# Performance work log

Hardware: AMD Instinct MI355X
Metric: run time of the kernel (lower is better)

## Reference

```python
import jax, jax.numpy as jnp
import numpy as np


def setup_inputs() -> dict:
    key = jax.random.key(0)
    k = jax.random.split(key, 4)
    B, F, E, U = 4096, 40, 64, 64
    return {
        "x": jax.random.normal(k[0], (B, F, E), dtype=jnp.float32),
        "attention_W": jax.random.normal(k[1], (E, U), dtype=jnp.float32) * (2.0 / (E + U)) ** 0.5,
        "attention_b": jnp.zeros((U,), dtype=jnp.float32),
        "projection_h": jax.random.normal(k[2], (U, 1), dtype=jnp.float32) * (2.0 / (U + 1)) ** 0.5,
        "projection_p": jax.random.normal(k[3], (E, 1), dtype=jnp.float32) * (2.0 / (E + 1)) ** 0.5,
    }


def reference(x, attention_W, attention_b, projection_h, projection_p):
    # x: [B, F, E] stacked field embeddings (original code takes a list of F [B,1,E])
    F = x.shape[1]
    ri, ci = np.triu_indices(F, k=1)  # static pair indices, P = F*(F-1)/2
    inner_product = x[:, ri, :] * x[:, ci, :]            # [B, P, E]
    attention_tmp = jax.nn.relu(
        jnp.einsum('bpe,eu->bpu', inner_product, attention_W) + attention_b
    )                                                    # [B, P, U]
    scores = jnp.einsum('bpu,uo->bpo', attention_tmp, projection_h)  # [B, P, 1]
    attention_weight = jax.nn.softmax(scores, axis=1)    # softmax over pairs
    attention_output = jnp.sum(inner_product * attention_weight, axis=1)  # [B, E]
    # dropout omitted (inference / eval mode)
    afm_out = attention_output @ projection_p            # [B, 1]
    return afm_out
```

## Files before the change

### kernel.cpp

```cpp
#include <hip/hip_runtime.h>
#include <hip/hip_fp16.h>

typedef _Float16 half8v __attribute__((ext_vector_type(8)));
typedef _Float16 half2v __attribute__((ext_vector_type(2)));
typedef float f32x4 __attribute__((ext_vector_type(4)));

#define DPP_XADD(x, ctrl)                                                          \
  x += __builtin_bit_cast(float, __builtin_amdgcn_mov_dpp(                         \
           __builtin_bit_cast(int, x), ctrl, 0xf, 0xf, true))

__global__ void afm_prep(const float* __restrict__ W, const float* __restrict__ pvec,
                         unsigned char* __restrict__ ws) {
  const int tid = threadIdx.x;
  _Float16* wf = (_Float16*)ws;
  _Float16* pf = (_Float16*)(ws + 8192);
  unsigned short* tbl = (unsigned short*)(ws + 10240);
  for (int idx = tid; idx < 4096; idx += 256) {
    int j = idx & 7, lane = (idx >> 3) & 63, nt = (idx >> 9) & 3, ks = idx >> 11;
    int k = ks * 32 + (lane >> 4) * 8 + j;
    int u = nt * 16 + (lane & 15);
    wf[idx] = (_Float16)W[k * 64 + u];
  }
  for (int idx = tid; idx < 1024; idx += 256) {
    int j = idx & 7, lane = (idx >> 3) & 63, ks = idx >> 9;
    int k = ks * 32 + (lane >> 4) * 8 + j;
    pf[idx] = ((lane & 15) == 0) ? (_Float16)pvec[k] : (_Float16)0.f;
  }
  for (int p = tid; p < 780; p += 256) {
    int i = 0, rem = p;
    while (rem >= 39 - i) { rem -= 39 - i; ++i; }
    int j = i + 1 + rem;
    tbl[p] = (unsigned short)((i << 8) | j);
  }
}

__global__ __launch_bounds__(256) void afm_main(
    const float* __restrict__ x, const float* __restrict__ bvec,
    const float* __restrict__ hvec, const unsigned char* __restrict__ ws,
    float* __restrict__ out) {
  __shared__ __align__(16) _Float16 xh[40 * 72];
  __shared__ __align__(16) unsigned short tbls[784];
  __shared__ float scs[784];
  __shared__ float s2s[784];
  __shared__ float red[12];

  const int tid = threadIdx.x;
  const int b = blockIdx.x;
  const int lane = tid & 63;
  const int wid = tid >> 6;

  const float4* xg = (const float4*)(x + b * 2560);
#pragma unroll
  for (int it = 0; it < 3; ++it) {
    int g = tid + it * 256;
    if (g < 640) {
      float4 v = xg[g];
      int f = g >> 4, e4 = g & 15;
      half2v* dst = (half2v*)&xh[f * 72 + e4 * 4];
      dst[0] = __builtin_bit_cast(half2v, __builtin_amdgcn_cvt_pkrtz(v.x, v.y));
      dst[1] = __builtin_bit_cast(half2v, __builtin_amdgcn_cvt_pkrtz(v.z, v.w));
    }
  }
  {
    const float4* tg = (const float4*)(ws + 10240);
    float4* ts = (float4*)tbls;
    if (tid < 98) ts[tid] = tg[tid];
  }
  const half8v* wfg = (const half8v*)ws;
  half8v wf[2][4];
#pragma unroll
  for (int ks = 0; ks < 2; ++ks)
#pragma unroll
    for (int nt = 0; nt < 4; ++nt) wf[ks][nt] = wfg[(ks * 4 + nt) * 64 + lane];
  const half8v* pfg = (const half8v*)(ws + 8192);
  half8v pf[2] = {pfg[lane], pfg[64 + lane]};
  float bu[4], hu[4];
#pragma unroll
  for (int nt = 0; nt < 4; ++nt) {
    int u = nt * 16 + (lane & 15);
    bu[nt] = bvec[u];
    hu[nt] = hvec[u];
  }
  __syncthreads();

  const int m = lane & 15, kg = lane >> 4;
  for (int t = wid; t < 49; t += 4) {
    int p = 16 * t + m;
    p = p > 779 ? 779 : p;
    unsigned pk = tbls[p];
    const _Float16* xi = &xh[(pk >> 8) * 72 + kg * 8];
    const _Float16* xj = &xh[(pk & 255) * 72 + kg * 8];
    half8v a0 = *(const half8v*)xi * *(const half8v*)xj;
    half8v a1 = *(const half8v*)(xi + 32) * *(const half8v*)(xj + 32);
    f32x4 acc[4], accp;
#pragma unroll
    for (int nt = 0; nt < 4; ++nt) acc[nt] = (f32x4){bu[nt], bu[nt], bu[nt], bu[nt]};
    accp = (f32x4){0.f, 0.f, 0.f, 0.f};
#pragma unroll
    for (int nt = 0; nt < 4; ++nt) {
      acc[nt] = __builtin_amdgcn_mfma_f32_16x16x32_f16(a0, wf[0][nt], acc[nt], 0, 0, 0);
      acc[nt] = __builtin_amdgcn_mfma_f32_16x16x32_f16(a1, wf[1][nt], acc[nt], 0, 0, 0);
    }
    accp = __builtin_amdgcn_mfma_f32_16x16x32_f16(a0, pf[0], accp, 0, 0, 0);
    accp = __builtin_amdgcn_mfma_f32_16x16x32_f16(a1, pf[1], accp, 0, 0, 0);
#pragma unroll
    for (int r = 0; r < 4; ++r) {
      float s = fmaxf(acc[0][r], 0.f) * hu[0] + fmaxf(acc[1][r], 0.f) * hu[1] +
                fmaxf(acc[2][r], 0.f) * hu[2] + fmaxf(acc[3][r], 0.f) * hu[3];
      DPP_XADD(s, 0xB1);
      DPP_XADD(s, 0x4E);
      DPP_XADD(s, 0x141);
      DPP_XADD(s, 0x140);
      int pr = 16 * t + kg * 4 + r;
      if (m == 0 && pr < 780) {
        scs[pr] = s;
        s2s[pr] = accp[r];
      }
    }
  }
  __syncthreads();

  float mx = -1e30f;
#pragma unroll
  for (int k2 = 0; k2 < 4; ++k2) {
    int p = tid + k2 * 256;
    if (p < 780) mx = fmaxf(mx, scs[p]);
  }
#pragma unroll
  for (int off = 32; off; off >>= 1) mx = fmaxf(mx, __shfl_xor(mx, off));
  if (lane == 0) red[wid] = mx;
  __syncthreads();
  mx = fmaxf(fmaxf(red[0], red[1]), fmaxf(red[2], red[3]));
  float num = 0.f, den = 0.f;
#pragma unroll
  for (int k2 = 0; k2 < 4; ++k2) {
    int p = tid + k2 * 256;
    if (p < 780) {
      float e = __expf(scs[p] - mx);
      num += e * s2s[p];
      den += e;
    }
  }
#pragma unroll
  for (int off = 32; off; off >>= 1) {
    num += __shfl_xor(num, off);
    den += __shfl_xor(den, off);
  }
  if (lane == 0) { red[4 + wid] = num; red[8 + wid] = den; }
  __syncthreads();
  if (tid == 0)
    out[b] = (red[4] + red[5] + red[6] + red[7]) /
             (red[8] + red[9] + red[10] + red[11]);
}

extern "C" void kernel_launch(void* const* d_in, const int* in_sizes, int n_in,
                              void* d_out, int out_size, void* d_ws, size_t ws_size,
                              hipStream_t stream) {
  const float* x    = (const float*)d_in[0];
  const float* W    = (const float*)d_in[1];
  const float* bvec = (const float*)d_in[2];
  const float* hvec = (const float*)d_in[3];
  const float* pvec = (const float*)d_in[4];
  float* out = (float*)d_out;
  unsigned char* ws = (unsigned char*)d_ws;

  hipLaunchKernelGGL(afm_prep, dim3(1), dim3(256), 0, stream, W, pvec, ws);
  hipLaunchKernelGGL(afm_main, dim3(4096), dim3(256), 0, stream, x, bvec, hvec, ws, out);
}
```

Measured before the change: 132.9 us.

## Fuse weight prep into main kernel and software-pipeline LDS pair reads

Removes the separate single-block prep kernel. Each block now loads W into shared memory, converts it into the fp16 MFMA operand layout, builds the pair table with a closed-form sqrt, and builds the projection operand itself. The pair loop is unrolled with double-buffered LDS reads so the next tile's x rows load while the current MFMAs run. The 16-lane DPP reduction is replaced by a partial-sum buffer in shared memory that is summed in the softmax phase. This saves a launch and its serialization, but adds per-block W staging, conversion work and more shared memory, which may lower occupancy.

```diff
diff --git a/kernel.cpp b/kernel.cpp
--- a/kernel.cpp
+++ b/kernel.cpp
@@ -9,45 +9,34 @@
   x += __builtin_bit_cast(float, __builtin_amdgcn_mov_dpp(                         \
            __builtin_bit_cast(int, x), ctrl, 0xf, 0xf, true))
 
-__global__ void afm_prep(const float* __restrict__ W, const float* __restrict__ pvec,
-                         unsigned char* __restrict__ ws) {
-  const int tid = threadIdx.x;
-  _Float16* wf = (_Float16*)ws;
-  _Float16* pf = (_Float16*)(ws + 8192);
-  unsigned short* tbl = (unsigned short*)(ws + 10240);
-  for (int idx = tid; idx < 4096; idx += 256) {
-    int j = idx & 7, lane = (idx >> 3) & 63, nt = (idx >> 9) & 3, ks = idx >> 11;
-    int k = ks * 32 + (lane >> 4) * 8 + j;
-    int u = nt * 16 + (lane & 15);
-    wf[idx] = (_Float16)W[k * 64 + u];
-  }
-  for (int idx = tid; idx < 1024; idx += 256) {
-    int j = idx & 7, lane = (idx >> 3) & 63, ks = idx >> 9;
-    int k = ks * 32 + (lane >> 4) * 8 + j;
-    pf[idx] = ((lane & 15) == 0) ? (_Float16)pvec[k] : (_Float16)0.f;
-  }
-  for (int p = tid; p < 780; p += 256) {
-    int i = 0, rem = p;
-    while (rem >= 39 - i) { rem -= 39 - i; ++i; }
-    int j = i + 1 + rem;
-    tbl[p] = (unsigned short)((i << 8) | j);
-  }
-}
-
-__global__ __launch_bounds__(256) void afm_main(
-    const float* __restrict__ x, const float* __restrict__ bvec,
-    const float* __restrict__ hvec, const unsigned char* __restrict__ ws,
-    float* __restrict__ out) {
+#define ISSUE_READS(slot, offw)                                                    \
+  do {                                                                             \
+    const _Float16* xi_ = &xh[((offw) >> 16) + eoff];                              \
+    const _Float16* xj_ = &xh[((offw) & 0xffffu) + eoff];                          \
+    xia[slot][0] = *(const half8v*)xi_;                                            \
+    xia[slot][1] = *(const half8v*)(xi_ + 32);                                     \
+    xja[slot][0] = *(const half8v*)xj_;                                            \
+    xja[slot][1] = *(const half8v*)(xj_ + 32);                                     \
+  } while (0)
+
+__global__ __launch_bounds__(256) void afm_fused(
+    const float* __restrict__ x, const float* __restrict__ W,
+    const float* __restrict__ bvec, const float* __restrict__ hvec,
+    const float* __restrict__ pvec, float* __restrict__ out) {
   __shared__ __align__(16) _Float16 xh[40 * 72];
-  __shared__ __align__(16) unsigned short tbls[784];
-  __shared__ float scs[784];
-  __shared__ float s2s[784];
+  __shared__ __align__(16) unsigned int tblu[784];
+  __shared__ __align__(16) float s2s[784];
   __shared__ float red[12];
+  __shared__ __align__(16) union WP {
+    float w[64 * 65];
+    float part[784 * 8];
+  } u;
 
   const int tid = threadIdx.x;
   const int b = blockIdx.x;
   const int lane = tid & 63;
   const int wid = tid >> 6;
+  const int m = lane & 15, kg = lane >> 4;
 
   const float4* xg = (const float4*)(x + b * 2560);
 #pragma unroll
@@ -61,90 +50,143 @@
       dst[1] = __builtin_bit_cast(half2v, __builtin_amdgcn_cvt_pkrtz(v.z, v.w));
     }
   }
+#pragma unroll
+  for (int it = 0; it < 4; ++it) {
+    int g = tid + it * 256;
+    float4 v = ((const float4*)W)[g];
+    int e = g >> 4, u4 = (g & 15) * 4;
+    float* dst = &u.w[e * 65 + u4];
+    dst[0] = v.x; dst[1] = v.y; dst[2] = v.z; dst[3] = v.w;
+  }
+  for (int p = tid; p < 784; p += 256) {
+    int pc = p > 779 ? 779 : p;
+    int i = (int)((79.0f - sqrtf(6241.0f - 8.0f * (float)pc)) * 0.5f);
+    i = i < 0 ? 0 : (i > 38 ? 38 : i);
+    while (i > 0 && (39 * i - (i * (i - 1)) / 2) > pc) --i;
+    while ((39 * (i + 1) - ((i + 1) * i) / 2) <= pc) ++i;
+    int base = 39 * i - (i * (i - 1)) / 2;
+    int j = i + 1 + (pc - base);
+    tblu[p] = ((unsigned)(i * 72) << 16) | (unsigned)(j * 72);
+  }
+  __syncthreads();
+
+  half8v wf[2][4];
+#pragma unroll
+  for (int ks = 0; ks < 2; ++ks)
+#pragma unroll
+    for (int nt = 0; nt < 4; ++nt) {
+      const float* src = &u.w[(ks * 32 + kg * 8) * 65 + nt * 16 + m];
+      half2v* hp = (half2v*)&wf[ks][nt];
+      hp[0] = __builtin_bit_cast(half2v, __builtin_amdgcn_cvt_pkrtz(src[0], src[65]));
+      hp[1] = __builtin_bit_cast(half2v, __builtin_amdgcn_cvt_pkrtz(src[130], src[195]));
+      hp[2] = __builtin_bit_cast(half2v, __builtin_amdgcn_cvt_pkrtz(src[260], src[325]));
+      hp[3] = __builtin_bit_cast(half2v, __builtin_amdgcn_cvt_pkrtz(src[390], src[455]));
+    }
+  half8v pf[2];
+#pragma unroll
+  for (int ks = 0; ks < 2; ++ks) {
+    half2v* hp = (half2v*)&pf[ks];
+#pragma unroll
+    for (int jj = 0; jj < 4; ++jj) {
+      int k = ks * 32 + kg * 8 + jj * 2;
+      float a = (m == 0) ? pvec[k] : 0.f;
+      float c = (m == 0) ? pvec[k + 1] : 0.f;
+      hp[jj] = __builtin_bit_cast(half2v, __builtin_amdgcn_cvt_pkrtz(a, c));
+    }
+  }
+  float bu[4], hu[4];
+#pragma unroll
+  for (int nt = 0; nt < 4; ++nt) {
+    int uu = nt * 16 + m;
+    bu[nt] = bvec[uu];
+    hu[nt] = hvec[uu];
+  }
+
+  const int eoff = kg * 8;
+  unsigned int off[2];
+  half8v xia[2][2], xja[2][2];
   {
-    const float4* tg = (const float4*)(ws + 10240);
-    float4* ts = (float4*)tbls;
-    if (tid < 98) ts[tid] = tg[tid];
-  }
-  const half8v* wfg = (const half8v*)ws;
-  half8v wf[2][4];
-#pragma unroll
-  for (int ks = 0; ks < 2; ++ks)
-#pragma unroll
-    for (int nt = 0; nt < 4; ++nt) wf[ks][nt] = wfg[(ks * 4 + nt) * 64 + lane];
-  const half8v* pfg = (const half8v*)(ws + 8192);
-  half8v pf[2] = {pfg[lane], pfg[64 + lane]};
-  float bu[4], hu[4];
-#pragma unroll
-  for (int nt = 0; nt < 4; ++nt) {
-    int u = nt * 16 + (lane & 15);
-    bu[nt] = bvec[u];
-    hu[nt] = hvec[u];
-  }
-  __syncthreads();
-
-  const int m = lane & 15, kg = lane >> 4;
-  for (int t = wid; t < 49; t += 4) {
-    int p = 16 * t + m;
-    p = p > 779 ? 779 : p;
-    unsigned pk = tbls[p];
-    const _Float16* xi = &xh[(pk >> 8) * 72 + kg * 8];
-    const _Float16* xj = &xh[(pk & 255) * 72 + kg * 8];
-    half8v a0 = *(const half8v*)xi * *(const half8v*)xj;
-    half8v a1 = *(const half8v*)(xi + 32) * *(const half8v*)(xj + 32);
-    f32x4 acc[4], accp;
-#pragma unroll
-    for (int nt = 0; nt < 4; ++nt) acc[nt] = (f32x4){bu[nt], bu[nt], bu[nt], bu[nt]};
-    accp = (f32x4){0.f, 0.f, 0.f, 0.f};
+    int p0 = 16 * wid + m;
+    off[0] = tblu[p0];
+    ISSUE_READS(0, off[0]);
+    int p1 = 16 * (wid + 4) + m;
+    p1 = p1 > 783 ? 783 : p1;
+    off[1] = tblu[p1];
+  }
+  __syncthreads();
+
+  float* part = u.part;
+#pragma unroll
+  for (int i = 0; i < 13; ++i) {
+    const int cur = i & 1, nxt = cur ^ 1;
+    if (i < 12) ISSUE_READS(nxt, off[nxt]);
+    if (i < 11) {
+      int pn = 16 * (wid + 4 * (i + 2)) + m;
+      pn = pn > 783 ? 783 : pn;
+      off[cur] = tblu[pn];
+    }
+    half8v a0 = xia[cur][0] * xja[cur][0];
+    half8v a1 = xia[cur][1] * xja[cur][1];
+    f32x4 acc[4];
 #pragma unroll
     for (int nt = 0; nt < 4; ++nt) {
+      acc[nt] = (f32x4){bu[nt], bu[nt], bu[nt], bu[nt]};
       acc[nt] = __builtin_amdgcn_mfma_f32_16x16x32_f16(a0, wf[0][nt], acc[nt], 0, 0, 0);
       acc[nt] = __builtin_amdgcn_mfma_f32_16x16x32_f16(a1, wf[1][nt], acc[nt], 0, 0, 0);
     }
+    f32x4 accp = (f32x4){0.f, 0.f, 0.f, 0.f};
     accp = __builtin_amdgcn_mfma_f32_16x16x32_f16(a0, pf[0], accp, 0, 0, 0);
     accp = __builtin_amdgcn_mfma_f32_16x16x32_f16(a1, pf[1], accp, 0, 0, 0);
+
+    const int t16 = 16 * (wid + 4 * i);
 #pragma unroll
     for (int r = 0; r < 4; ++r) {
       float s = fmaxf(acc[0][r], 0.f) * hu[0] + fmaxf(acc[1][r], 0.f) * hu[1] +
                 fmaxf(acc[2][r], 0.f) * hu[2] + fmaxf(acc[3][r], 0.f) * hu[3];
       DPP_XADD(s, 0xB1);
-      DPP_XADD(s, 0x4E);
-      DPP_XADD(s, 0x141);
-      DPP_XADD(s, 0x140);
-      int pr = 16 * t + kg * 4 + r;
-      if (m == 0 && pr < 780) {
-        scs[pr] = s;
-        s2s[pr] = accp[r];
+      int pr = t16 + kg * 4 + r;
+      if (pr < 780) {
+        if ((m & 1) == 0) part[pr * 8 + (m >> 1)] = s;
+        if (m == 0) s2s[pr] = accp[r];
       }
     }
   }
   __syncthreads();
 
+  float sv[4];
   float mx = -1e30f;
-#pragma unroll
-  for (int k2 = 0; k2 < 4; ++k2) {
-    int p = tid + k2 * 256;
-    if (p < 780) mx = fmaxf(mx, scs[p]);
-  }
-#pragma unroll
-  for (int off = 32; off; off >>= 1) mx = fmaxf(mx, __shfl_xor(mx, off));
-  if (lane == 0) red[wid] = mx;
-  __syncthreads();
-  mx = fmaxf(fmaxf(red[0], red[1]), fmaxf(red[2], red[3]));
-  float num = 0.f, den = 0.f;
 #pragma unroll
   for (int k2 = 0; k2 < 4; ++k2) {
     int p = tid + k2 * 256;
     if (p < 780) {
-      float e = __expf(scs[p] - mx);
+      const f32x4* pp = (const f32x4*)&part[p * 8];
+      f32x4 lo = pp[0], hi = pp[1];
+      float s = ((lo[0] + lo[1]) + (lo[2] + lo[3])) + ((hi[0] + hi[1]) + (hi[2] + hi[3]));
+      sv[k2] = s;
+      mx = fmaxf(mx, s);
+    } else {
+      sv[k2] = -1e30f;
+    }
+  }
+#pragma unroll
+  for (int o = 32; o; o >>= 1) mx = fmaxf(mx, __shfl_xor(mx, o));
+  if (lane == 0) red[wid] = mx;
+  __syncthreads();
+  mx = fmaxf(fmaxf(red[0], red[1]), fmaxf(red[2], red[3]));
+  float num = 0.f, den = 0.f;
+#pragma unroll
+  for (int k2 = 0; k2 < 4; ++k2) {
+    int p = tid + k2 * 256;
+    if (p < 780) {
+      float e = __expf(sv[k2] - mx);
       num += e * s2s[p];
       den += e;
     }
   }
 #pragma unroll
-  for (int off = 32; off; off >>= 1) {
-    num += __shfl_xor(num, off);
-    den += __shfl_xor(den, off);
+  for (int o = 32; o; o >>= 1) {
+    num += __shfl_xor(num, o);
+    den += __shfl_xor(den, o);
   }
   if (lane == 0) { red[4 + wid] = num; red[8 + wid] = den; }
   __syncthreads();
@@ -162,8 +204,7 @@
   const float* hvec = (const float*)d_in[3];
   const float* pvec = (const float*)d_in[4];
   float* out = (float*)d_out;
-  unsigned char* ws = (unsigned char*)d_ws;
-
-  hipLaunchKernelGGL(afm_prep, dim3(1), dim3(256), 0, stream, W, pvec, ws);
-  hipLaunchKernelGGL(afm_main, dim3(4096), dim3(256), 0, stream, x, bvec, hvec, ws, out);
+
+  hipLaunchKernelGGL(afm_fused, dim3(4096), dim3(256), 0, stream,
+                     x, W, bvec, hvec, pvec, out);
 }
```

Measured after the change: 143.2 us. 7.8% more time.
